# Performance work log

Measured on AMD Instinct MI355X. Metric: run time of the kernel, lower is better.

The kernel has to match this reference:

```python
import jax, jax.numpy as jnp
import numpy as np

# Cylinder3D-like first encoder stage
B, D, H, W = 1, 480, 360, 32      # batch and dense voxel grid (z, y, x)
N = 200000                        # active voxels
CIN, COUT = 32, 64
SLOPE = 0.01                      # nn.LeakyReLU default negative_slope
STRIDE, PAD, K = 2, 1, 3          # SparseConv3d pool params
DO, HO, WO = 240, 180, 16         # (D+2*PAD-K)//STRIDE + 1 per dim

# kernel (3,1,3): taps along z and x; kernel (1,3,3): taps along y and x
OFF_31 = [(dz, 0, dx) for dz in (-1, 0, 1) for dx in (-1, 0, 1)]
OFF_13 = [(0, dy, dx) for dy in (-1, 0, 1) for dx in (-1, 0, 1)]


def setup_inputs() -> dict:
    rng = np.random.default_rng(0)
    # unique active voxel coordinates (submanifold semantics require uniqueness)
    lin = rng.choice(B * D * H * W, size=N, replace=False)
    b = lin // (D * H * W)
    r = lin % (D * H * W)
    z = r // (H * W)
    r = r % (H * W)
    y = r // W
    x = r % W
    coords = jnp.asarray(np.stack([b, z, y, x], axis=1).astype(np.int32))
    ks = jax.random.split(jax.random.key(0), 6)
    sc = 0.05
    return {
        "feats": jax.random.normal(ks[0], (N, CIN), jnp.float32),
        "coords": coords,
        "W1": jax.random.normal(ks[1], (9, CIN, COUT), jnp.float32) * sc,
        "W1_2": jax.random.normal(ks[2], (9, COUT, COUT), jnp.float32) * sc,
        "W2": jax.random.normal(ks[3], (9, CIN, COUT), jnp.float32) * sc,
        "W3": jax.random.normal(ks[4], (9, COUT, COUT), jnp.float32) * sc,
        "Wpool": jax.random.normal(ks[5], (27, COUT, COUT), jnp.float32) * sc,
    }


def _leaky(v):
    return jnp.where(v > 0, v, SLOPE * v)


def _table(coords):
    # dense voxel -> point-index map, -1 == empty
    lin = ((coords[:, 0] * D + coords[:, 1]) * H + coords[:, 2]) * W + coords[:, 3]
    return jnp.full((B * D * H * W,), -1, jnp.int32).at[lin].set(jnp.arange(N, dtype=jnp.int32))


def _subm(feat, coords, table, Wk, offsets):
    # submanifold conv: gather active neighbors, GEMM per tap, accumulate at same sites
    out = jnp.zeros((feat.shape[0], Wk.shape[2]), feat.dtype)
    bz, z, y, x = coords[:, 0], coords[:, 1], coords[:, 2], coords[:, 3]
    for k, (dz, dy, dx) in enumerate(offsets):
        nz, ny, nx = z + dz, y + dy, x + dx
        inb = (nz >= 0) & (nz < D) & (ny >= 0) & (ny < H) & (nx >= 0) & (nx < W)
        nlin = ((bz * D + jnp.clip(nz, 0, D - 1)) * H + jnp.clip(ny, 0, H - 1)) * W + jnp.clip(nx, 0, W - 1)
        nidx = table[nlin]
        ok = inb & (nidx >= 0)
        g = jnp.where(ok[:, None], feat[jnp.where(ok, nidx, 0)], 0.0)
        out = out + g @ Wk[k]
    return out


def _pool(feat, coords, Wp):
    # strided SparseConv3d scattered into the dense downsampled grid;
    # values at spconv-active output sites match spconv, inactive sites are 0
    dense = jnp.zeros((B * DO * HO * WO, Wp.shape[2]), feat.dtype)
    bz, z, y, x = coords[:, 0], coords[:, 1], coords[:, 2], coords[:, 3]
    k = 0
    for kd in range(K):
        for kh in range(K):
            for kw in range(K):
                oz, oy, ox = z + PAD - kd, y + PAD - kh, x + PAD - kw
                ok = (oz % STRIDE == 0) & (oy % STRIDE == 0) & (ox % STRIDE == 0)
                oz, oy, ox = oz // STRIDE, oy // STRIDE, ox // STRIDE
                ok = ok & (oz >= 0) & (oz < DO) & (oy >= 0) & (oy < HO) & (ox >= 0) & (ox < WO)
                olin = jnp.where(ok, ((bz * DO + oz) * HO + oy) * WO + ox, 0)
                dense = dense.at[olin].add((feat @ Wp[k]) * ok[:, None])
                k += 1
    return dense.reshape(B, DO, HO, WO, Wp.shape[2])


def reference(feats, coords, W1, W1_2, W2, W3, Wpool):
    table = _table(coords)
    # shortcut branch: conv3x1 -> LeakyReLU -> conv1x3 -> LeakyReLU
    sc = _leaky(_subm(feats, coords, table, W1, OFF_31))
    sc = _leaky(_subm(sc, coords, table, W1_2, OFF_13))
    # main branch: conv1x3 -> LeakyReLU -> conv3x1 -> LeakyReLU
    rA = _leaky(_subm(feats, coords, table, W2, OFF_13))
    rA = _leaky(_subm(rA, coords, table, W3, OFF_31))
    rA = rA + sc                      # residual add on .features
    pooled = _pool(rA, coords, Wpool)  # stride-2 SparseConv3d downsample
    return pooled, rA
```

## Files before the change

kernel.cpp:

```cpp
#include <hip/hip_runtime.h>
#include <stdint.h>

#define D_  480
#define H_  360
#define W_  32
#define N_  200000
#define DO_ 240
#define HO_ 180
#define WO_ 16
#define NCELL (DO_*HO_*WO_)
#define NVOX  (D_*H_*W_)
#define HBITS 19
#define HSZ   (1<<HBITS)
#define HMASK (HSZ-1)
#define CAPC 16384
#define CAPP 32768
#define CSTRIDE 32

#define PBZ_CELLS 32768
#define POOL_BLOCKS 512
#define POOL_WAVES (POOL_BLOCKS*4)
#define PB_PER_WAVE (PBZ_CELLS/POOL_WAVES)

__device__ __forceinline__ float bf2f(uint16_t u){
  uint32_t x=((uint32_t)u)<<16; return __builtin_bit_cast(float,x);
}
__device__ __forceinline__ uint16_t f2bf(float f){
  uint32_t x=__builtin_bit_cast(uint32_t,f);
  uint32_t r=x+0x7fffu+((x>>16)&1u);
  return (uint16_t)(r>>16);
}
template<bool F32> __device__ __forceinline__ float ldv(const void* p,size_t i){
  if constexpr(F32) return ((const float*)p)[i];
  else return bf2f(((const uint16_t*)p)[i]);
}
template<bool F32> __device__ __forceinline__ void stv(void* p,size_t i,float v){
  if constexpr(F32) ((float*)p)[i]=v;
  else ((uint16_t*)p)[i]=f2bf(v);
}
template<bool F32> __device__ __forceinline__ void ld8(const void* p,size_t base,float* v){
  if constexpr(F32){
    const float4* q=(const float4*)((const float*)p+base);
    float4 a=q[0], b=q[1];
    v[0]=a.x;v[1]=a.y;v[2]=a.z;v[3]=a.w;
    v[4]=b.x;v[5]=b.y;v[6]=b.z;v[7]=b.w;
  }else{
    const uint4* q=(const uint4*)((const uint16_t*)p+base);
    uint4 a=q[0];
    v[0]=bf2f((uint16_t)(a.x&0xffffu)); v[1]=bf2f((uint16_t)(a.x>>16));
    v[2]=bf2f((uint16_t)(a.y&0xffffu)); v[3]=bf2f((uint16_t)(a.y>>16));
    v[4]=bf2f((uint16_t)(a.z&0xffffu)); v[5]=bf2f((uint16_t)(a.z>>16));
    v[6]=bf2f((uint16_t)(a.w&0xffffu)); v[7]=bf2f((uint16_t)(a.w>>16));
  }
}
__device__ __forceinline__ float rlane(float v,int l){
  return __builtin_bit_cast(float,
      __builtin_amdgcn_readlane(__builtin_bit_cast(int,v),l));
}
__device__ __forceinline__ float lk(float v){ return v>0.f? v:0.01f*v; }

__device__ __forceinline__ uint32_t hash0(int lin){
  return ((uint32_t)((uint32_t)lin*2654435761u)>>12)&HMASK;
}
__device__ __forceinline__ int hlookup(const int2* __restrict__ h,int lin){
  uint32_t s=hash0(lin);
  for(;;){ int2 kv=h[s]; if(kv.x==lin) return kv.y; if(kv.x<0) return -1; s=(s+1)&HMASK; }
}

__global__ void k_sniff(const uint16_t* __restrict__ feats,int* __restrict__ flag){
  __shared__ int s;
  if(threadIdx.x==0) s=0;
  __syncthreads();
  int bad=0;
  for(int i=threadIdx.x;i<512;i+=256){
    int e=(feats[i]>>7)&0xff;
    bad += (e>=0x90)?1:0;
  }
  atomicAdd(&s,bad);
  if(threadIdx.x<45) flag[128+threadIdx.x*CSTRIDE]=0;
  __syncthreads();
  if(threadIdx.x==0){ flag[0]=(s>=8)?1:0; flag[1]=0; }
}

__global__ void k_table_init(int* __restrict__ t){
  int i=blockIdx.x*256+threadIdx.x;
  if(i<NVOX/4) ((int4*)t)[i]=make_int4(-1,-1,-1,-1);
}
__global__ void k_table_build(const int4* __restrict__ coords,int* __restrict__ t){
  int i=blockIdx.x*256+threadIdx.x;
  if(i>=N_) return;
  int4 c=coords[i];
  t[(c.y*H_+c.z)*W_+c.w]=i;
}

__global__ void k_hash_init(int2* __restrict__ h){
  int i=blockIdx.x*256+threadIdx.x;
  if(i<HSZ) h[i]=make_int2(-1,-1);
}
__global__ void k_hash_build(const int4* __restrict__ coords,int2* __restrict__ h){
  int i=blockIdx.x*256+threadIdx.x;
  if(i>=N_) return;
  int4 c=coords[i];
  int lin=(c.y*H_+c.z)*W_+c.w;
  uint32_t s=hash0(lin);
  for(;;){
    int old=atomicCAS(&h[s].x,-1,lin);
    if(old==-1){ h[s].y=i; break; }
    s=(s+1)&HMASK;
  }
}


__device__ __forceinline__ void wappend(int2* __restrict__ lst,int* __restrict__ cnt,
                                        int cap,int a,int b,bool want,int lane){
  unsigned long long m=__ballot(want);
  if(m==0ull) return;
  int first=__builtin_ctzll(m);
  int base=0;
  if(lane==first) base=atomicAdd(cnt,__popcll(m));
  base=__shfl(base,first);
  if(want){
    int pref=__popcll(m&((1ull<<lane)-1ull));
    int pos=base+pref;
    if(pos<cap) lst[pos]=make_int2(a,b);
  }
}

__global__ __launch_bounds__(256)
void k_build_conv(const int4* __restrict__ coords,const int* __restrict__ table,
                  int2* __restrict__ listA,int2* __restrict__ listB,
                  int* __restrict__ cntA,int* __restrict__ cntB,
                  const int* __restrict__ flag){
  if(!flag[0]) return;
  int i=blockIdx.x*256+threadIdx.x;
  bool valid=i<N_;
  int4 c = valid? coords[i] : make_int4(0,0,0,0);
  int z=c.y,y=c.z,x=c.w;
  int lane=threadIdx.x&63;
  #pragma unroll
  for(int j=0;j<9;j++){
    int k=(blockIdx.x+j)%9;
    if(k==4) continue;
    int d0=k/3-1, dx=k%3-1;
    {
      int nz=z+d0, nx=x+dx;
      int src=-1;
      if(valid && nz>=0&&nz<D_&&nx>=0&&nx<W_) src=table[(nz*H_+y)*W_+nx];
      wappend(listA+(size_t)k*CAPC,&cntA[k*CSTRIDE],CAPC,i,src,src>=0,lane);
    }
    {
      int ny=y+d0, nx=x+dx;
      int src=-1;
      if(valid && ny>=0&&ny<H_&&nx>=0&&nx<W_) src=table[(z*H_+ny)*W_+nx];
      wappend(listB+(size_t)k*CAPC,&cntB[k*CSTRIDE],CAPC,i,src,src>=0,lane);
    }
  }
}

__global__ __launch_bounds__(256)
void k_build_pool(const int4* __restrict__ coords,int2* __restrict__ listP,
                  int* __restrict__ cntP,const int* __restrict__ flag){
  if(!flag[0]) return;
  int i=blockIdx.x*256+threadIdx.x;
  bool valid=i<N_;
  int4 c = valid? coords[i] : make_int4(0,0,0,0);
  int z=c.y,y=c.z,x=c.w;
  int lane=threadIdx.x&63;
  #pragma unroll
  for(int j=0;j<27;j++){
    int k=(blockIdx.x+j)%27;
    int kd=k/9, kh=(k/3)%3, kw=k%3;
    int tz=z+1-kd, ty=y+1-kh, tx=x+1-kw;
    bool ok = valid && !(tz&1)&&!(ty&1)&&!(tx&1);
    int oz=tz>>1, oy=ty>>1, ox=tx>>1;
    ok = ok && oz>=0&&oz<DO_&&oy>=0&&oy<HO_&&ox>=0&&ox<WO_;
    int cell = ok? ((oz*HO_+oy)*WO_+ox) : -1;
    wappend(listP+(size_t)k*CAPP,&cntP[k*CSTRIDE],CAPP,cell,i,ok,lane);
  }
}

template<int CIN,bool ACT>
__global__ __launch_bounds__(256,1)
void k_center(const float* __restrict__ src,const float* __restrict__ Wl,
              float* __restrict__ dst,const int* __restrict__ flag){
  if(!flag[0]) return;
  int wave=blockIdx.x*4+(threadIdx.x>>6);
  int lane=threadIdx.x&63;
  int p0=wave*4;
  if(p0>=N_) return;
  float w[CIN];
  #pragma unroll
  for(int ci=0;ci<CIN;ci++) w[ci]=Wl[(size_t)4*CIN*64+(size_t)ci*64+lane];
  int li=(CIN==64)? lane : (lane&31);
  float r0=src[(size_t)(p0+0)*CIN+li];
  float r1=src[(size_t)(p0+1)*CIN+li];
  float r2=src[(size_t)(p0+2)*CIN+li];
  float r3=src[(size_t)(p0+3)*CIN+li];
  if(ACT){ r0=lk(r0); r1=lk(r1); r2=lk(r2); r3=lk(r3); }
  float a0=0.f,a1=0.f,a2=0.f,a3=0.f;
  #pragma unroll
  for(int ci=0;ci<CIN;ci++){
    float wc=w[ci];
    a0+=rlane(r0,ci)*wc; a1+=rlane(r1,ci)*wc;
    a2+=rlane(r2,ci)*wc; a3+=rlane(r3,ci)*wc;
  }
  dst[(size_t)(p0+0)*64+lane]=a0;
  dst[(size_t)(p0+1)*64+lane]=a1;
  dst[(size_t)(p0+2)*64+lane]=a2;
  dst[(size_t)(p0+3)*64+lane]=a3;
}

template<int CIN,bool ACT>
__global__ __launch_bounds__(256,1)
void k_off(const float* __restrict__ src,const float* __restrict__ Wl,
           const int2* __restrict__ lists,const int* __restrict__ cnt,
           float* __restrict__ dst,const int* __restrict__ flag){
  if(!flag[0]) return;
  int g=blockIdx.y;
  if(g==4) return;
  int n=min(cnt[g*CSTRIDE],CAPC);
  const int2* lst=lists+(size_t)g*CAPC;
  int wave=blockIdx.x*4+(threadIdx.x>>6);
  int lane=threadIdx.x&63;
  float w[CIN];
  #pragma unroll
  for(int ci=0;ci<CIN;ci++) w[ci]=Wl[(size_t)g*CIN*64+(size_t)ci*64+lane];
  int nw=gridDim.x*4;
  int li=(CIN==64)? lane : (lane&31);
  for(int p=wave;p<n;p+=nw){
    int2 pr=lst[p];
    float r=src[(size_t)pr.y*CIN+li];
    if(ACT) r=lk(r);
    float a=0.f;
    #pragma unroll
    for(int ci=0;ci<CIN;ci++) a+=rlane(r,ci)*w[ci];
    atomicAdd(&dst[(size_t)pr.x*64+lane],a);
  }
}

__global__ __launch_bounds__(256,1)
void k_pools(const float* __restrict__ rAp,const float* __restrict__ Wp,
             const int2* __restrict__ listP,const int* __restrict__ cntP,
             float* __restrict__ out,const int* __restrict__ flag){
  if(!flag[0]) return;
  int g=blockIdx.y;
  int n=min(cntP[g*CSTRIDE],CAPP);
  const int2* lst=listP+(size_t)g*CAPP;
  int wave=blockIdx.x*4+(threadIdx.x>>6);
  int lane=threadIdx.x&63;
  float w[64];
  #pragma unroll
  for(int ci=0;ci<64;ci++) w[ci]=Wp[(size_t)g*4096+(size_t)ci*64+lane];
  int nw=gridDim.x*4;
  for(int p0=wave*4;p0<n;p0+=nw*4){
    int pB=p0+1,pC=p0+2,pD=p0+3;
    bool vB=pB<n, vC=pC<n, vD=pD<n;
    int2 qA=lst[p0];
    int2 qB=vB?lst[pB]:qA;
    int2 qC=vC?lst[pC]:qA;
    int2 qD=vD?lst[pD]:qA;
    float rA_=rAp[(size_t)qA.y*64+lane];
    float rB_=rAp[(size_t)qB.y*64+lane];
    float rC_=rAp[(size_t)qC.y*64+lane];
    float rD_=rAp[(size_t)qD.y*64+lane];
    float aA=0.f,aB=0.f,aC=0.f,aD=0.f;
    #pragma unroll
    for(int ci=0;ci<64;ci++){
      float wc=w[ci];
      aA+=rlane(rA_,ci)*wc;
      aB+=rlane(rB_,ci)*wc;
      aC+=rlane(rC_,ci)*wc;
      aD+=rlane(rD_,ci)*wc;
    }
    atomicAdd(&out[(size_t)qA.x*64+lane],aA);
    if(vB) atomicAdd(&out[(size_t)qB.x*64+lane],aB);
    if(vC) atomicAdd(&out[(size_t)qC.x*64+lane],aC);
    if(vD) atomicAdd(&out[(size_t)qD.x*64+lane],aD);
  }
}

__global__ __launch_bounds__(256)
void k_act_resid(float* __restrict__ r,const float* __restrict__ sc,
                 const int* __restrict__ flag){
  if(!flag[0]) return;
  size_t n=(size_t)N_*64;
  size_t stride=(size_t)gridDim.x*1024;
  for(size_t i=((size_t)blockIdx.x*256+threadIdx.x)*4;i<n;i+=stride){
    float4 v=*(float4*)(r+i);
    float4 s=*(const float4*)(sc+i);
    v.x=lk(v.x)+lk(s.x); v.y=lk(v.y)+lk(s.y);
    v.z=lk(v.z)+lk(s.z); v.w=lk(v.w)+lk(s.w);
    *(float4*)(r+i)=v;
  }
}
__global__ __launch_bounds__(256)
void k_zero(float* __restrict__ out,const int* __restrict__ flag){
  if(!flag[0]) return;
  size_t n=(size_t)NCELL*64;
  size_t stride=(size_t)gridDim.x*1024;
  float4 z=make_float4(0.f,0.f,0.f,0.f);
  for(size_t i=((size_t)blockIdx.x*256+threadIdx.x)*4;i<n;i+=stride)
    *(float4*)(out+i)=z;
}

template<int CIN,bool AXIS31,int SRC,int DST,bool RESID>
__global__ __launch_bounds__(256)
void k_convb(const void* __restrict__ feats,const int4* __restrict__ coords,
             const int* __restrict__ table,const void* __restrict__ Wk,
             char* __restrict__ ob,const int* __restrict__ flag){
  if(flag[0]) return;
  uint16_t* buf0=(uint16_t*)ob;
  uint16_t* buf1=buf0+(size_t)N_*64;
  int wave=blockIdx.x*4+(threadIdx.x>>6);
  int lane=threadIdx.x&63;
  if(wave>=N_) return;
  int4 c=coords[wave];
  int z=c.y,y=c.z,x=c.w;
  int nidx=-1;
  if(lane<9){
    int d0=lane/3-1, dxo=lane%3-1;
    int nz=AXIS31? z+d0:z;
    int ny=AXIS31? y:y+d0;
    int nx=x+dxo;
    if(nz>=0&&nz<D_&&ny>=0&&ny<H_&&nx>=0&&nx<W_)
      nidx=table[(nz*H_+ny)*W_+nx];
  }
  unsigned long long m=__ballot(nidx>=0);
  float acc=0.f;
  while(m){
    int k=__builtin_ctzll(m); m&=m-1;
    int idx=__shfl(nidx,k);
    size_t fb=(size_t)idx*CIN;
    size_t wb=(size_t)k*CIN*64+lane;
    #pragma unroll
    for(int g=0;g<CIN/8;g++){
      float f[8];
      if(SRC==0) ld8<false>(feats,fb+(size_t)8*g,f);
      else       ld8<false>(buf0 ,fb+(size_t)8*g,f);
      #pragma unroll
      for(int j=0;j<8;j++)
        acc+=f[j]*ldv<false>(Wk,wb+(size_t)(8*g+j)*64);
    }
  }
  float v=acc>0.f? acc:0.01f*acc;
  if(RESID) v+=bf2f(buf1[(size_t)wave*64+lane]);
  size_t oi=(size_t)wave*64+lane;
  if(DST==0)      buf0[oi]=f2bf(v);
  else if(DST==1) buf1[oi]=f2bf(v);
  else            stv<false>(ob+(size_t)NCELL*64*2,oi,v);
}

__global__ __launch_bounds__(256)
void k_poolb(const int* __restrict__ table,const void* __restrict__ Wp,
             char* __restrict__ ob,const int* __restrict__ flag){
  if(flag[0]) return;
  const char* rAp=ob+(size_t)NCELL*64*2;
  int wave=blockIdx.x*4+(threadIdx.x>>6);
  int lane=threadIdx.x&63;
  int cell0=wave*2;
  if(cell0>=NCELL) return;
  int half=lane>>5, l=lane&31;
  int cell=cell0+half;
  int ox=cell&(WO_-1);
  int t=cell>>4;
  int oy=t%HO_, oz=t/HO_;
  int nidx=-1;
  if(l<27){
    int kd=l/9, kh=(l/3)%3, kw=l%3;
    int z=2*oz+kd-1, y=2*oy+kh-1, x=2*ox+kw-1;
    if(z>=0&&z<D_&&y>=0&&y<H_&&x>=0&&x<W_)
      nidx=table[(z*H_+y)*W_+x];
  }
  unsigned long long m=__ballot(nidx>=0);
  unsigned int ma=(unsigned int)(m&0x07FFFFFFull);
  unsigned int mb=(unsigned int)((m>>32)&0x07FFFFFFull);
  float acc0=0.f, acc1=0.f;
  while(ma|mb){
    int ka=-1,kb=-1,ia=0,ib=0;
    if(ma){ ka=__builtin_ctz(ma); ma&=ma-1; ia=__shfl(nidx,ka); }
    if(mb){ kb=__builtin_ctz(mb); mb&=mb-1; ib=__shfl(nidx,32+kb); }
    if(ka>=0){
      size_t fb=(size_t)ia*64, wb=(size_t)ka*4096+lane;
      #pragma unroll
      for(int g=0;g<8;g++){
        float f[8]; ld8<false>(rAp,fb+(size_t)8*g,f);
        #pragma unroll
        for(int j=0;j<8;j++) acc0+=f[j]*ldv<false>(Wp,wb+(size_t)(8*g+j)*64);
      }
    }
    if(kb>=0){
      size_t fb=(size_t)ib*64, wb=(size_t)kb*4096+lane;
      #pragma unroll
      for(int g=0;g<8;g++){
        float f[8]; ld8<false>(rAp,fb+(size_t)8*g,f);
        #pragma unroll
        for(int j=0;j<8;j++) acc1+=f[j]*ldv<false>(Wp,wb+(size_t)(8*g+j)*64);
      }
    }
  }
  stv<false>(ob,(size_t)cell0*64+lane,acc0);
  stv<false>(ob,((size_t)cell0+1)*64+lane,acc1);
}

template<int CIN,bool AXIS31,int SRC,int DST,bool RESID,bool F32>
__device__ __forceinline__ void conv_body(const void* __restrict__ feats,
                                          const int4* __restrict__ coords,
                                          const int2* __restrict__ hash,
                                          const void* __restrict__ Wk,
                                          char* __restrict__ ob){
  constexpr size_t ESZ=F32?4:2;
  uint16_t* buf0=(uint16_t*)(ob+(size_t)PBZ_CELLS*64*ESZ);
  uint16_t* buf1=buf0+(size_t)N_*64;
  int wave=blockIdx.x*4+(threadIdx.x>>6);
  int lane=threadIdx.x&63;
  if(wave>=N_) return;
  int4 c=coords[wave];
  int z=c.y,y=c.z,x=c.w;
  float acc=0.f;
  #pragma unroll
  for(int k=0;k<9;k++){
    const int d0=k/3-1, dxo=k%3-1;
    int nz=AXIS31? z+d0:z;
    int ny=AXIS31? y:y+d0;
    int nx=x+dxo;
    int nidx=-1;
    if(nz>=0&&nz<D_&&ny>=0&&ny<H_&&nx>=0&&nx<W_)
      nidx=hlookup(hash,(nz*H_+ny)*W_+nx);
    nidx=__builtin_amdgcn_readfirstlane(nidx);
    if(nidx<0) continue;
    size_t fb=(size_t)nidx*CIN;
    size_t wb=(size_t)k*CIN*64+lane;
    #pragma unroll
    for(int ci=0;ci<CIN;ci+=2){
      float f0=(SRC==0)? ldv<F32>(feats,fb+ci)   : bf2f(buf0[fb+ci]);
      float f1=(SRC==0)? ldv<F32>(feats,fb+ci+1) : bf2f(buf0[fb+ci+1]);
      acc += f0*ldv<F32>(Wk,wb+(size_t)ci*64);
      acc += f1*ldv<F32>(Wk,wb+(size_t)(ci+1)*64);
    }
  }
  float v=acc>0.f? acc:0.01f*acc;
  if(RESID) v+=bf2f(buf1[(size_t)wave*64+lane]);
  size_t oi=(size_t)wave*64+lane;
  if(DST==0)      buf0[oi]=f2bf(v);
  else if(DST==1) buf1[oi]=f2bf(v);
  else            stv<F32>(ob+(size_t)NCELL*64*ESZ,oi,v);
}
template<int CIN,bool AXIS31,int SRC,int DST,bool RESID>
__global__ __launch_bounds__(256)
void k_conv(const void* feats,const int4* coords,const int2* hash,const void* Wk,
            char* ob,const int* flag){
  if(flag[0]) conv_body<CIN,AXIS31,SRC,DST,RESID,true >(feats,coords,hash,Wk,ob);
  else        conv_body<CIN,AXIS31,SRC,DST,RESID,false>(feats,coords,hash,Wk,ob);
}
template<bool F32>
__device__ __forceinline__ float pool_cell_t(int cell,const void* __restrict__ rA,
    const int2* __restrict__ hash,const void* __restrict__ Wp,int lane){
  int ox=cell&(WO_-1);
  int t=cell>>4;
  int oy=t%HO_, oz=t/HO_;
  float acc=0.f;
  int k=0;
  for(int kd=0;kd<3;kd++)for(int kh=0;kh<3;kh++)for(int kw=0;kw<3;kw++,k++){
    int z=2*oz+kd-1, y=2*oy+kh-1, x=2*ox+kw-1;
    if(z<0||z>=D_||y<0||y>=H_||x<0||x>=W_) continue;
    int nidx=hlookup(hash,(z*H_+y)*W_+x);
    nidx=__builtin_amdgcn_readfirstlane(nidx);
    if(nidx<0) continue;
    size_t fb=(size_t)nidx*64;
    size_t wb=(size_t)k*4096+lane;
    #pragma unroll
    for(int ci=0;ci<64;ci+=2){
      acc+=ldv<F32>(rA,fb+ci)  *ldv<F32>(Wp,wb+(size_t)ci*64);
      acc+=ldv<F32>(rA,fb+ci+1)*ldv<F32>(Wp,wb+(size_t)(ci+1)*64);
    }
  }
  return acc;
}
template<bool F32>
__device__ __forceinline__ void pool_fb_body(const void* __restrict__ Wp,
                                             char* __restrict__ ob,
                                             int* __restrict__ cnt){
  constexpr size_t ESZ=F32?4:2;
  const int2* hash=(const int2*)ob;
  const void* rA=ob+(size_t)NCELL*64*ESZ;
  int w=blockIdx.x*4+(threadIdx.x>>6);
  int lane=threadIdx.x&63;
  for(int cell=PBZ_CELLS+w; cell<NCELL; cell+=POOL_WAVES)
    stv<F32>(ob,(size_t)cell*64+lane, pool_cell_t<F32>(cell,rA,hash,Wp,lane));
  float accb[PB_PER_WAVE];
  #pragma unroll
  for(int j=0;j<PB_PER_WAVE;j++)
    accb[j]=pool_cell_t<F32>(w*PB_PER_WAVE+j,rA,hash,Wp,lane);
  __syncthreads();
  if(threadIdx.x==0){
    __threadfence();
    atomicAdd(cnt,1);
    while(atomicAdd(cnt,0)<POOL_BLOCKS) __builtin_amdgcn_s_sleep(8);
  }
  __syncthreads();
  #pragma unroll
  for(int j=0;j<PB_PER_WAVE;j++)
    stv<F32>(ob,(size_t)(w*PB_PER_WAVE+j)*64+lane,accb[j]);
}
__global__ __launch_bounds__(256,2)
void k_pool_fb(const void* Wp,char* ob,int* cnt,const int* flag){
  if(flag[0]) pool_fb_body<true >(Wp,ob,cnt);
  else        pool_fb_body<false>(Wp,ob,cnt);
}

extern "C" void kernel_launch(void* const* d_in,const int* in_sizes,int n_in,
                              void* d_out,int out_size,void* d_ws,size_t ws_size,
                              hipStream_t stream){
  const uint16_t* feats_u16=(const uint16_t*)d_in[0];
  const void* feats=d_in[0];
  const int4* coords=(const int4*)d_in[1];
  const void* W1  =d_in[2];
  const void* W1_2=d_in[3];
  const void* W2  =d_in[4];
  const void* W3  =d_in[5];
  const void* Wp  =d_in[6];
  char* ob=(char*)d_out;
  int* flag=(int*)d_ws;

  const size_t OFF_TABLE=8192;
  const size_t OFF_LISTA=OFF_TABLE+(size_t)NVOX*4;
  const size_t OFF_LISTB=OFF_LISTA+(size_t)9*CAPC*8;
  const size_t OFF_LISTP=OFF_LISTB+(size_t)9*CAPC*8;
  const size_t WS_NEED  =OFF_LISTP+(size_t)27*CAPP*8;
  const bool ws_ok = ws_size >= WS_NEED;

  int* cnt =flag+128;
  int* cntA=cnt, *cntB=cnt+9*CSTRIDE, *cntP=cnt+18*CSTRIDE;
  int*  table=(int*)((char*)d_ws+OFF_TABLE);
  int2* listA=(int2*)((char*)d_ws+OFF_LISTA);
  int2* listB=(int2*)((char*)d_ws+OFF_LISTB);
  int2* listP=(int2*)((char*)d_ws+OFF_LISTP);

  float* bufA=(float*)ob;
  float* bufB=(float*)(ob+(size_t)N_*64*4);
  float* rAf =(float*)(ob+(size_t)NCELL*64*4);

  k_sniff<<<1,256,0,stream>>>(feats_u16,flag);

  if(ws_ok){
    k_table_init <<<NVOX/4/256,256,0,stream>>>(table);
    k_table_build<<<(N_+255)/256,256,0,stream>>>(coords,table);
    k_build_conv <<<(N_+255)/256,256,0,stream>>>(coords,table,listA,listB,cntA,cntB,flag);
    k_build_pool <<<(N_+255)/256,256,0,stream>>>(coords,listP,cntP,flag);

    const float* W1f  =(const float*)W1;
    const float* W12f =(const float*)W1_2;
    const float* W2f  =(const float*)W2;
    const float* W3f  =(const float*)W3;
    const float* Wpf  =(const float*)Wp;
    const float* featsf=(const float*)feats;

    k_center<32,false><<<N_/16,256,0,stream>>>(featsf,W1f,bufA,flag);
    k_off<32,false><<<dim3(64,9),256,0,stream>>>(featsf,W1f,listA,cntA,bufA,flag);
    k_center<64,true ><<<N_/16,256,0,stream>>>(bufA,W12f,bufB,flag);
    k_off<64,true ><<<dim3(64,9),256,0,stream>>>(bufA,W12f,listB,cntB,bufB,flag);
    k_center<32,false><<<N_/16,256,0,stream>>>(featsf,W2f,bufA,flag);
    k_off<32,false><<<dim3(64,9),256,0,stream>>>(featsf,W2f,listB,cntB,bufA,flag);
    k_center<64,true ><<<N_/16,256,0,stream>>>(bufA,W3f,rAf,flag);
    k_off<64,true ><<<dim3(64,9),256,0,stream>>>(bufA,W3f,listA,cntA,rAf,flag);
    k_act_resid<<<2048,256,0,stream>>>(rAf,bufB,flag);
    k_zero<<<4096,256,0,stream>>>((float*)ob,flag);
    k_pools<<<dim3(128,27),256,0,stream>>>(rAf,Wpf,listP,cntP,(float*)ob,flag);

    k_convb<32,true ,0,0,false><<<N_/4,256,0,stream>>>(feats,coords,table,W1  ,ob,flag);
    k_convb<64,false,1,1,false><<<N_/4,256,0,stream>>>(feats,coords,table,W1_2,ob,flag);
    k_convb<32,false,0,0,false><<<N_/4,256,0,stream>>>(feats,coords,table,W2  ,ob,flag);
    k_convb<64,true ,1,2,true ><<<N_/4,256,0,stream>>>(feats,coords,table,W3  ,ob,flag);
    k_poolb<<<NCELL/8,256,0,stream>>>(table,Wp,ob,flag);
  }else{
    int2* hash=(int2*)ob;
    k_hash_init<<<(HSZ+255)/256,256,0,stream>>>(hash);
    k_hash_build<<<(N_+255)/256,256,0,stream>>>(coords,hash);
    k_conv<32,true ,0,0,false><<<N_/4,256,0,stream>>>(feats,coords,hash,W1  ,ob,flag);
    k_conv<64,false,1,1,false><<<N_/4,256,0,stream>>>(feats,coords,hash,W1_2,ob,flag);
    k_conv<32,false,0,0,false><<<N_/4,256,0,stream>>>(feats,coords,hash,W2  ,ob,flag);
    k_conv<64,true ,1,2,true ><<<N_/4,256,0,stream>>>(feats,coords,hash,W3  ,ob,flag);
    k_pool_fb<<<POOL_BLOCKS,256,0,stream>>>(Wp,ob,flag+1,flag);
  }
}
```

Measured before the change: 957.9 us.

## Merge list builders, widen per-wave point batches, skip unused dtype path

Merges the conv and pool neighbor-list builders into a single kernel and replaces the zeroing kernel with hipMemsetAsync. The center kernel now handles 8 points per wave and the offset kernel 2 pairs per wave, with weights held in 16-wide vector registers. The host reads the feature input size to pick the f32 or bf16 path and skips launching the other one. Larger per-wave batches raise register pressure, and the dtype check assumes in_sizes is reliable.

```diff
diff --git a/kernel.cpp b/kernel.cpp
--- a/kernel.cpp
+++ b/kernel.cpp
@@ -22,6 +22,8 @@
 #define POOL_WAVES (POOL_BLOCKS*4)
 #define PB_PER_WAVE (PBZ_CELLS/POOL_WAVES)
 
+typedef float f32x16 __attribute__((ext_vector_type(16)));
+
 __device__ __forceinline__ float bf2f(uint16_t u){
   uint32_t x=((uint32_t)u)<<16; return __builtin_bit_cast(float,x);
 }
@@ -59,6 +61,27 @@
 }
 __device__ __forceinline__ float lk(float v){ return v>0.f? v:0.01f*v; }
 
+template<int CIN> struct WR { f32x16 v[CIN/16]; };
+template<int CIN>
+__device__ __forceinline__ void wload(WR<CIN>& w,const float* __restrict__ Wt,int lane){
+  #pragma unroll
+  for(int j=0;j<CIN/16;j++)
+    #pragma unroll
+    for(int i=0;i<16;i++)
+      w.v[j][i]=Wt[(size_t)(j*16+i)*64+lane];
+}
+template<int CIN,int R>
+__device__ __forceinline__ void wdotR(float* a,const float* r,const WR<CIN>& w){
+  #pragma unroll
+  for(int j=0;j<CIN/16;j++)
+    #pragma unroll
+    for(int i=0;i<16;i++){
+      float wc=w.v[j][i];
+      #pragma unroll
+      for(int q=0;q<R;q++) a[q]+=rlane(r[q],j*16+i)*wc;
+    }
+}
+
 __device__ __forceinline__ uint32_t hash0(int lin){
   return ((uint32_t)((uint32_t)lin*2654435761u)>>12)&HMASK;
 }
@@ -127,10 +150,11 @@
 }
 
 __global__ __launch_bounds__(256)
-void k_build_conv(const int4* __restrict__ coords,const int* __restrict__ table,
-                  int2* __restrict__ listA,int2* __restrict__ listB,
-                  int* __restrict__ cntA,int* __restrict__ cntB,
-                  const int* __restrict__ flag){
+void k_build(const int4* __restrict__ coords,const int* __restrict__ table,
+             int2* __restrict__ listA,int2* __restrict__ listB,
+             int2* __restrict__ listP,
+             int* __restrict__ cntA,int* __restrict__ cntB,int* __restrict__ cntP,
+             const int* __restrict__ flag){
   if(!flag[0]) return;
   int i=blockIdx.x*256+threadIdx.x;
   bool valid=i<N_;
@@ -155,17 +179,6 @@
       wappend(listB+(size_t)k*CAPC,&cntB[k*CSTRIDE],CAPC,i,src,src>=0,lane);
     }
   }
-}
-
-__global__ __launch_bounds__(256)
-void k_build_pool(const int4* __restrict__ coords,int2* __restrict__ listP,
-                  int* __restrict__ cntP,const int* __restrict__ flag){
-  if(!flag[0]) return;
-  int i=blockIdx.x*256+threadIdx.x;
-  bool valid=i<N_;
-  int4 c = valid? coords[i] : make_int4(0,0,0,0);
-  int z=c.y,y=c.z,x=c.w;
-  int lane=threadIdx.x&63;
   #pragma unroll
   for(int j=0;j<27;j++){
     int k=(blockIdx.x+j)%27;
@@ -186,28 +199,21 @@
   if(!flag[0]) return;
   int wave=blockIdx.x*4+(threadIdx.x>>6);
   int lane=threadIdx.x&63;
-  int p0=wave*4;
+  int p0=wave*8;
   if(p0>=N_) return;
-  float w[CIN];
-  #pragma unroll
-  for(int ci=0;ci<CIN;ci++) w[ci]=Wl[(size_t)4*CIN*64+(size_t)ci*64+lane];
+  WR<CIN> w;
+  wload<CIN>(w,Wl+(size_t)4*CIN*64,lane);
   int li=(CIN==64)? lane : (lane&31);
-  float r0=src[(size_t)(p0+0)*CIN+li];
-  float r1=src[(size_t)(p0+1)*CIN+li];
-  float r2=src[(size_t)(p0+2)*CIN+li];
-  float r3=src[(size_t)(p0+3)*CIN+li];
-  if(ACT){ r0=lk(r0); r1=lk(r1); r2=lk(r2); r3=lk(r3); }
-  float a0=0.f,a1=0.f,a2=0.f,a3=0.f;
-  #pragma unroll
-  for(int ci=0;ci<CIN;ci++){
-    float wc=w[ci];
-    a0+=rlane(r0,ci)*wc; a1+=rlane(r1,ci)*wc;
-    a2+=rlane(r2,ci)*wc; a3+=rlane(r3,ci)*wc;
-  }
-  dst[(size_t)(p0+0)*64+lane]=a0;
-  dst[(size_t)(p0+1)*64+lane]=a1;
-  dst[(size_t)(p0+2)*64+lane]=a2;
-  dst[(size_t)(p0+3)*64+lane]=a3;
+  float r[8],a[8];
+  #pragma unroll
+  for(int q=0;q<8;q++){
+    r[q]=src[(size_t)(p0+q)*CIN+li];
+    if(ACT) r[q]=lk(r[q]);
+    a[q]=0.f;
+  }
+  wdotR<CIN,8>(a,r,w);
+  #pragma unroll
+  for(int q=0;q<8;q++) dst[(size_t)(p0+q)*64+lane]=a[q];
 }
 
 template<int CIN,bool ACT>
@@ -222,19 +228,23 @@
   const int2* lst=lists+(size_t)g*CAPC;
   int wave=blockIdx.x*4+(threadIdx.x>>6);
   int lane=threadIdx.x&63;
-  float w[CIN];
-  #pragma unroll
-  for(int ci=0;ci<CIN;ci++) w[ci]=Wl[(size_t)g*CIN*64+(size_t)ci*64+lane];
+  WR<CIN> w;
+  wload<CIN>(w,Wl+(size_t)g*CIN*64,lane);
   int nw=gridDim.x*4;
   int li=(CIN==64)? lane : (lane&31);
-  for(int p=wave;p<n;p+=nw){
-    int2 pr=lst[p];
-    float r=src[(size_t)pr.y*CIN+li];
-    if(ACT) r=lk(r);
-    float a=0.f;
-    #pragma unroll
-    for(int ci=0;ci<CIN;ci++) a+=rlane(r,ci)*w[ci];
-    atomicAdd(&dst[(size_t)pr.x*64+lane],a);
+  for(int p0=wave*2;p0<n;p0+=nw*2){
+    int p1=p0+1;
+    bool v1=p1<n;
+    int2 qA=lst[p0];
+    int2 qB=v1?lst[p1]:qA;
+    float r[2],a[2];
+    r[0]=src[(size_t)qA.y*CIN+li];
+    r[1]=src[(size_t)qB.y*CIN+li];
+    if(ACT){ r[0]=lk(r[0]); r[1]=lk(r[1]); }
+    a[0]=0.f; a[1]=0.f;
+    wdotR<CIN,2>(a,r,w);
+    atomicAdd(&dst[(size_t)qA.x*64+lane],a[0]);
+    if(v1) atomicAdd(&dst[(size_t)qB.x*64+lane],a[1]);
   }
 }
 
@@ -248,9 +258,8 @@
   const int2* lst=listP+(size_t)g*CAPP;
   int wave=blockIdx.x*4+(threadIdx.x>>6);
   int lane=threadIdx.x&63;
-  float w[64];
-  #pragma unroll
-  for(int ci=0;ci<64;ci++) w[ci]=Wp[(size_t)g*4096+(size_t)ci*64+lane];
+  WR<64> w;
+  wload<64>(w,Wp+(size_t)g*4096,lane);
   int nw=gridDim.x*4;
   for(int p0=wave*4;p0<n;p0+=nw*4){
     int pB=p0+1,pC=p0+2,pD=p0+3;
@@ -259,23 +268,17 @@
     int2 qB=vB?lst[pB]:qA;
     int2 qC=vC?lst[pC]:qA;
     int2 qD=vD?lst[pD]:qA;
-    float rA_=rAp[(size_t)qA.y*64+lane];
-    float rB_=rAp[(size_t)qB.y*64+lane];
-    float rC_=rAp[(size_t)qC.y*64+lane];
-    float rD_=rAp[(size_t)qD.y*64+lane];
-    float aA=0.f,aB=0.f,aC=0.f,aD=0.f;
-    #pragma unroll
-    for(int ci=0;ci<64;ci++){
-      float wc=w[ci];
-      aA+=rlane(rA_,ci)*wc;
-      aB+=rlane(rB_,ci)*wc;
-      aC+=rlane(rC_,ci)*wc;
-      aD+=rlane(rD_,ci)*wc;
-    }
-    atomicAdd(&out[(size_t)qA.x*64+lane],aA);
-    if(vB) atomicAdd(&out[(size_t)qB.x*64+lane],aB);
-    if(vC) atomicAdd(&out[(size_t)qC.x*64+lane],aC);
-    if(vD) atomicAdd(&out[(size_t)qD.x*64+lane],aD);
+    float r[4],a[4];
+    r[0]=rAp[(size_t)qA.y*64+lane];
+    r[1]=rAp[(size_t)qB.y*64+lane];
+    r[2]=rAp[(size_t)qC.y*64+lane];
+    r[3]=rAp[(size_t)qD.y*64+lane];
+    a[0]=0.f;a[1]=0.f;a[2]=0.f;a[3]=0.f;
+    wdotR<64,4>(a,r,w);
+    atomicAdd(&out[(size_t)qA.x*64+lane],a[0]);
+    if(vB) atomicAdd(&out[(size_t)qB.x*64+lane],a[1]);
+    if(vC) atomicAdd(&out[(size_t)qC.x*64+lane],a[2]);
+    if(vD) atomicAdd(&out[(size_t)qD.x*64+lane],a[3]);
   }
 }
 
@@ -292,15 +295,6 @@
     v.z=lk(v.z)+lk(s.z); v.w=lk(v.w)+lk(s.w);
     *(float4*)(r+i)=v;
   }
-}
-__global__ __launch_bounds__(256)
-void k_zero(float* __restrict__ out,const int* __restrict__ flag){
-  if(!flag[0]) return;
-  size_t n=(size_t)NCELL*64;
-  size_t stride=(size_t)gridDim.x*1024;
-  float4 z=make_float4(0.f,0.f,0.f,0.f);
-  for(size_t i=((size_t)blockIdx.x*256+threadIdx.x)*4;i<n;i+=stride)
-    *(float4*)(out+i)=z;
 }
 
 template<int CIN,bool AXIS31,int SRC,int DST,bool RESID>
@@ -522,6 +516,12 @@
   char* ob=(char*)d_out;
   int* flag=(int*)d_ws;
 
+  const long fbytes=in_sizes? (long)in_sizes[0] : -1;
+  const bool h_f32  = fbytes==(long)N_*32*4;
+  const bool h_bf16 = fbytes==(long)N_*32*2;
+  const bool run_f32  = h_f32  || !(h_f32||h_bf16);
+  const bool run_bf16 = h_bf16 || !(h_f32||h_bf16);
+
   const size_t OFF_TABLE=8192;
   const size_t OFF_LISTA=OFF_TABLE+(size_t)NVOX*4;
   const size_t OFF_LISTB=OFF_LISTA+(size_t)9*CAPC*8;
@@ -545,33 +545,37 @@
   if(ws_ok){
     k_table_init <<<NVOX/4/256,256,0,stream>>>(table);
     k_table_build<<<(N_+255)/256,256,0,stream>>>(coords,table);
-    k_build_conv <<<(N_+255)/256,256,0,stream>>>(coords,table,listA,listB,cntA,cntB,flag);
-    k_build_pool <<<(N_+255)/256,256,0,stream>>>(coords,listP,cntP,flag);
-
-    const float* W1f  =(const float*)W1;
-    const float* W12f =(const float*)W1_2;
-    const float* W2f  =(const float*)W2;
-    const float* W3f  =(const float*)W3;
-    const float* Wpf  =(const float*)Wp;
-    const float* featsf=(const float*)feats;
-
-    k_center<32,false><<<N_/16,256,0,stream>>>(featsf,W1f,bufA,flag);
-    k_off<32,false><<<dim3(64,9),256,0,stream>>>(featsf,W1f,listA,cntA,bufA,flag);
-    k_center<64,true ><<<N_/16,256,0,stream>>>(bufA,W12f,bufB,flag);
-    k_off<64,true ><<<dim3(64,9),256,0,stream>>>(bufA,W12f,listB,cntB,bufB,flag);
-    k_center<32,false><<<N_/16,256,0,stream>>>(featsf,W2f,bufA,flag);
-    k_off<32,false><<<dim3(64,9),256,0,stream>>>(featsf,W2f,listB,cntB,bufA,flag);
-    k_center<64,true ><<<N_/16,256,0,stream>>>(bufA,W3f,rAf,flag);
-    k_off<64,true ><<<dim3(64,9),256,0,stream>>>(bufA,W3f,listA,cntA,rAf,flag);
-    k_act_resid<<<2048,256,0,stream>>>(rAf,bufB,flag);
-    k_zero<<<4096,256,0,stream>>>((float*)ob,flag);
-    k_pools<<<dim3(128,27),256,0,stream>>>(rAf,Wpf,listP,cntP,(float*)ob,flag);
-
-    k_convb<32,true ,0,0,false><<<N_/4,256,0,stream>>>(feats,coords,table,W1  ,ob,flag);
-    k_convb<64,false,1,1,false><<<N_/4,256,0,stream>>>(feats,coords,table,W1_2,ob,flag);
-    k_convb<32,false,0,0,false><<<N_/4,256,0,stream>>>(feats,coords,table,W2  ,ob,flag);
-    k_convb<64,true ,1,2,true ><<<N_/4,256,0,stream>>>(feats,coords,table,W3  ,ob,flag);
-    k_poolb<<<NCELL/8,256,0,stream>>>(table,Wp,ob,flag);
+
+    if(run_f32){
+      k_build<<<(N_+255)/256,256,0,stream>>>(coords,table,listA,listB,listP,
+                                             cntA,cntB,cntP,flag);
+      const float* W1f  =(const float*)W1;
+      const float* W12f =(const float*)W1_2;
+      const float* W2f  =(const float*)W2;
+      const float* W3f  =(const float*)W3;
+      const float* Wpf  =(const float*)Wp;
+      const float* featsf=(const float*)feats;
+
+      k_center<32,false><<<N_/32,256,0,stream>>>(featsf,W1f,bufA,flag);
+      k_off<32,false><<<dim3(64,9),256,0,stream>>>(featsf,W1f,listA,cntA,bufA,flag);
+      k_center<64,true ><<<N_/32,256,0,stream>>>(bufA,W12f,bufB,flag);
+      k_off<64,true ><<<dim3(64,9),256,0,stream>>>(bufA,W12f,listB,cntB,bufB,flag);
+      k_center<32,false><<<N_/32,256,0,stream>>>(featsf,W2f,bufA,flag);
+      k_off<32,false><<<dim3(64,9),256,0,stream>>>(featsf,W2f,listB,cntB,bufA,flag);
+      k_center<64,true ><<<N_/32,256,0,stream>>>(bufA,W3f,rAf,flag);
+      k_off<64,true ><<<dim3(64,9),256,0,stream>>>(bufA,W3f,listA,cntA,rAf,flag);
+      k_act_resid<<<2048,256,0,stream>>>(rAf,bufB,flag);
+      hipMemsetAsync((void*)ob,0,(size_t)NCELL*64*4,stream);
+      k_pools<<<dim3(128,27),256,0,stream>>>(rAf,Wpf,listP,cntP,(float*)ob,flag);
+    }
+
+    if(run_bf16){
+      k_convb<32,true ,0,0,false><<<N_/4,256,0,stream>>>(feats,coords,table,W1  ,ob,flag);
+      k_convb<64,false,1,1,false><<<N_/4,256,0,stream>>>(feats,coords,table,W1_2,ob,flag);
+      k_convb<32,false,0,0,false><<<N_/4,256,0,stream>>>(feats,coords,table,W2  ,ob,flag);
+      k_convb<64,true ,1,2,true ><<<N_/4,256,0,stream>>>(feats,coords,table,W3  ,ob,flag);
+      k_poolb<<<NCELL/8,256,0,stream>>>(table,Wp,ob,flag);
+    }
   }else{
     int2* hash=(int2*)ob;
     k_hash_init<<<(HSZ+255)/256,256,0,stream>>>(hash);
```

After: 912.3 us. 1.05x faster.
